# Performance work log

Measured on AMD Instinct MI355X. Metric: run time of the kernel, lower is better.

## Reference

```python
import jax, jax.numpy as jnp
import numpy as np

B, T, U = 4, 500, 100
D = 512   # d_model
H = 512   # d_hidden
L = 2     # num_layers
V = 64    # len(phonemes)


def setup_inputs() -> dict:
    key = jax.random.key(0)
    ks = jax.random.split(key, 14)
    g = lambda k, shp: (jax.random.normal(k, shp, jnp.float32) * 0.05)
    return {
        "input_ids": jax.random.randint(ks[0], (B, U), 0, V),
        "memory": jax.random.normal(ks[1], (B, T, D), jnp.float32),
        "emb": g(ks[2], (V, D)),
        # stacked per-layer LSTM params (torch layout: [4H, in], gate order i,f,g,o)
        "w_ih": g(ks[3], (L, 4 * H, D)),
        "w_hh": g(ks[4], (L, 4 * H, H)),
        "b_ih": g(ks[5], (L, 4 * H)),
        "b_hh": g(ks[6], (L, 4 * H)),
        "fc_w": g(ks[7], (D, H)),     # torch Linear [out, in]
        "fc_b": g(ks[8], (D,)),
        "jw1": g(ks[9], (H, 2 * D)),  # Joint.forward_layer
        "jb1": g(ks[10], (H,)),
        "jw2": g(ks[11], (V, H)),     # Joint.project_layer
        "jb2": g(ks[12], (V,)),
    }


def _lstm_layer(x, wi, wh, bi, bh):
    # x: [B, U, in] -> returns ([B, U, H], h_T [B,H], c_T [B,H])
    b = x.shape[0]
    h0 = jnp.zeros((b, H), x.dtype)
    c0 = jnp.zeros((b, H), x.dtype)
    bias = bi + bh

    def step(carry, xt):
        h, c = carry
        gates = xt @ wi.T + h @ wh.T + bias  # [B, 4H]
        i, f, g, o = jnp.split(gates, 4, axis=-1)
        c = jax.nn.sigmoid(f) * c + jax.nn.sigmoid(i) * jnp.tanh(g)
        h = jax.nn.sigmoid(o) * jnp.tanh(c)
        return (h, c), h

    (hT, cT), ys = jax.lax.scan(step, (h0, c0), jnp.swapaxes(x, 0, 1))
    return jnp.swapaxes(ys, 0, 1), hT, cT


def reference(input_ids, memory, emb, w_ih, w_hh, b_ih, b_hh, fc_w, fc_b, jw1, jb1, jw2, jb2):
    # embedding lookup
    x = emb[input_ids]  # [B, U, D]
    hs, cs = [], []
    for l in range(L):
        x, hT, cT = _lstm_layer(x, w_ih[l], w_hh[l], b_ih[l], b_hh[l])
        hs.append(hT)
        cs.append(cT)
    h = jnp.stack(hs)  # [L, B, H]
    c = jnp.stack(cs)
    x = x @ fc_w.T + fc_b  # [B, U, D]

    # Joint: linear over concat(enc, dec) == split-weight broadcast add (same math)
    we = jw1[:, :D]  # acts on enc_state
    wd = jw1[:, D:]  # acts on dec_state
    enc_p = jnp.einsum("btd,hd->bth", memory, we)  # [B, T, H]
    dec_p = jnp.einsum("bud,hd->buh", x, wd)       # [B, U, H]
    joint_h = jnp.tanh(enc_p[:, :, None, :] + dec_p[:, None, :, :] + jb1)  # [B,T,U,H]
    out = jnp.einsum("btuh,vh->btuv", joint_h, jw2) + jb2  # [B, T, U, V]
    return out, h, c
```

## Files before the change

### kernel.cpp

```cpp
#include <hip/hip_runtime.h>

#define Bc 4
#define Tc 500
#define Uc 100
#define Vc 64
#define G4 2048

typedef __attribute__((ext_vector_type(8))) short short8v;
typedef __attribute__((ext_vector_type(4))) float f32x4;
typedef _Float16 h2v __attribute__((ext_vector_type(2)));

#define SMEM_BYTES 86016

__device__ __forceinline__ float fsig(float x) {
  return __builtin_amdgcn_rcpf(1.f + __expf(-x));
}
__device__ __forceinline__ float ftanh(float x) {
  float e = __expf(2.f * x);
  return 1.f - 2.f * __builtin_amdgcn_rcpf(e + 1.f);
}
__device__ __forceinline__ short f2bf(float f) {
  unsigned u = __float_as_uint(f);
  unsigned r = (u + 0x7FFFu + ((u >> 16) & 1u)) >> 16;
  return (short)r;
}

__device__ __forceinline__ unsigned ldA(const unsigned* p) {
  return __hip_atomic_load(p, __ATOMIC_RELAXED, __HIP_MEMORY_SCOPE_AGENT);
}
__device__ __forceinline__ void stA(unsigned* p, unsigned v) {
  __hip_atomic_store(p, v, __ATOMIC_RELAXED, __HIP_MEMORY_SCOPE_AGENT);
}

template <int ATOMICST>
__device__ __forceinline__ void gemm_tile(
    char* smem,
    const float* __restrict__ A, int lda,
    const float* __restrict__ Bw, int ldb,
    const float* __restrict__ bias, const float* __restrict__ bias2,
    float* __restrict__ C, int ldc, int N, int m0, int n0,
    const int* __restrict__ ids, const float* __restrict__ emb)
{
  float (*As)[65] = (float (*)[65])smem;
  float (*Bs)[65] = (float (*)[65])(smem + 4160);
  const int tid = threadIdx.x;
  const int tx = tid & 15, ty = tid >> 4;
  float acc[4][4] = {};
  for (int k0 = 0; k0 < 512; k0 += 16) {
#pragma unroll
    for (int i = 0; i < 4; ++i) {
      int n = n0 + ty + 16 * i;
      float av = 0.f;
      if (n < N) {
        const float* ar = ids ? (emb + (long)ids[n] * 512) : (A + (long)n * lda);
        av = ar[k0 + tx];
      }
      As[tx][ty + 16 * i] = av;
      Bs[tx][ty + 16 * i] = Bw[(long)(m0 + ty + 16 * i) * ldb + k0 + tx];
    }
    __syncthreads();
#pragma unroll
    for (int kl = 0; kl < 16; ++kl) {
      float a[4], b[4];
#pragma unroll
      for (int i = 0; i < 4; ++i) a[i] = As[kl][ty * 4 + i];
#pragma unroll
      for (int j = 0; j < 4; ++j) b[j] = Bs[kl][tx * 4 + j];
#pragma unroll
      for (int i = 0; i < 4; ++i)
#pragma unroll
        for (int j = 0; j < 4; ++j) acc[i][j] += a[i] * b[j];
    }
    __syncthreads();
  }
#pragma unroll
  for (int i = 0; i < 4; ++i) {
    int n = n0 + ty * 4 + i;
    if (n >= N) continue;
#pragma unroll
    for (int j = 0; j < 4; ++j) {
      int m = m0 + tx * 4 + j;
      float v = acc[i][j];
      if (bias)  v += bias[m];
      if (bias2) v += bias2[m];
      if (ATOMICST)
        stA((unsigned*)C + (long)n * ldc + m, __float_as_uint(v));
      else
        C[(long)n * ldc + m] = v;
    }
  }
}

__device__ void wdc_tile(char* smem,
                         const float* __restrict__ jw1,
                         const float* __restrict__ fc_w,
                         float* __restrict__ wdc, int n0, int m0)
{
  float (*As)[65] = (float (*)[65])smem;
  float (*Bs)[65] = (float (*)[65])(smem + 4160);
  const int tid = threadIdx.x;
  const int tx = tid & 15, ty = tid >> 4;
  float acc[4][4] = {};
  for (int k0 = 0; k0 < 512; k0 += 16) {
#pragma unroll
    for (int i = 0; i < 4; ++i) {
      As[tx][ty + 16 * i] = jw1[(long)(n0 + ty + 16 * i) * 1024 + 512 + k0 + tx];
      Bs[ty][tx + 16 * i] = fc_w[(long)(k0 + ty) * 512 + m0 + tx + 16 * i];
    }
    __syncthreads();
#pragma unroll
    for (int kl = 0; kl < 16; ++kl) {
      float a[4], b[4];
#pragma unroll
      for (int i = 0; i < 4; ++i) a[i] = As[kl][ty * 4 + i];
#pragma unroll
      for (int j = 0; j < 4; ++j) b[j] = Bs[kl][tx * 4 + j];
#pragma unroll
      for (int i = 0; i < 4; ++i)
#pragma unroll
        for (int j = 0; j < 4; ++j) acc[i][j] += a[i] * b[j];
    }
    __syncthreads();
  }
#pragma unroll
  for (int i = 0; i < 4; ++i)
#pragma unroll
    for (int j = 0; j < 4; ++j)
      stA((unsigned*)wdc + (long)(n0 + ty * 4 + i) * 512 + m0 + tx * 4 + j,
          __float_as_uint(acc[i][j]));
}

__device__ void dec_tile(char* smem,
                         const float* __restrict__ h1s, const float* __restrict__ wdc,
                         const float* __restrict__ jw1, const float* __restrict__ fc_b,
                         const float* __restrict__ jb1, float* __restrict__ decb,
                         const int* __restrict__ f1, int m0, int n0)
{
  float (*As)[65] = (float (*)[65])smem;
  float (*Bs)[65] = (float (*)[65])(smem + 4160);
  float* biasl = (float*)(smem + 8320);
  const int tid = threadIdx.x;
  const int tx = tid & 15, ty = tid >> 4;
  int u_hi = 0;
  for (int rr = 0; rr < 64; ++rr) {
    int r = n0 + rr;
    if (r < 400) { int u = r % Uc; u_hi = max(u_hi, u + 1); }
  }
  if (tid < 32)
    while ((int)ldA((const unsigned*)(f1 + tid * 16)) < u_hi)
      __builtin_amdgcn_s_sleep(8);
  if (tid < 64) {
    int m = m0 + tid;
    const float4* wp = (const float4*)(jw1 + (long)m * 1024 + 512);
    const float4* fb = (const float4*)fc_b;
    float bb = jb1[m];
#pragma unroll 8
    for (int d4 = 0; d4 < 128; ++d4) {
      float4 w = wp[d4], f = fb[d4];
      bb += w.x * f.x + w.y * f.y + w.z * f.z + w.w * f.w;
    }
    biasl[tid] = bb;
  }
  __syncthreads();
  const unsigned* h1u = (const unsigned*)h1s;
  const unsigned* wdu = (const unsigned*)wdc;
  float acc[4][4] = {};
  for (int k0 = 0; k0 < 512; k0 += 16) {
    unsigned uA[4], uB[4];
#pragma unroll
    for (int i = 0; i < 4; ++i) {
      int n = n0 + ty + 16 * i;
      uA[i] = (n < 400) ? ldA(h1u + (long)(n % Uc) * G4 + (n / Uc) * 512 + k0 + tx) : 0u;
      uB[i] = ldA(wdu + (long)(m0 + ty + 16 * i) * 512 + k0 + tx);
    }
#pragma unroll
    for (int i = 0; i < 4; ++i) {
      int n = n0 + ty + 16 * i;
      while (uA[i] == 0xFFFFFFFFu)
        uA[i] = ldA(h1u + (long)(n % Uc) * G4 + (n / Uc) * 512 + k0 + tx);
      while (uB[i] == 0xFFFFFFFFu)
        uB[i] = ldA(wdu + (long)(m0 + ty + 16 * i) * 512 + k0 + tx);
      As[tx][ty + 16 * i] = __uint_as_float(uA[i]);
      Bs[tx][ty + 16 * i] = __uint_as_float(uB[i]);
    }
    __syncthreads();
#pragma unroll
    for (int kl = 0; kl < 16; ++kl) {
      float a[4], b[4];
#pragma unroll
      for (int i = 0; i < 4; ++i) a[i] = As[kl][ty * 4 + i];
#pragma unroll
      for (int j = 0; j < 4; ++j) b[j] = Bs[kl][tx * 4 + j];
#pragma unroll
      for (int i = 0; i < 4; ++i)
#pragma unroll
        for (int j = 0; j < 4; ++j) acc[i][j] += a[i] * b[j];
    }
    __syncthreads();
  }
#pragma unroll
  for (int i = 0; i < 4; ++i) {
    int n = n0 + ty * 4 + i;
    if (n >= 400) continue;
#pragma unroll
    for (int j = 0; j < 4; ++j)
      stA((unsigned*)decb + (long)n * 512 + m0 + tx * 4 + j,
          __float_as_uint(acc[i][j] + biasl[tx * 4 + j]));
  }
}

__device__ void rec_path(
    char* smem, int role,
    const float* __restrict__ ixp0,
    const float* __restrict__ wih1, const float* __restrict__ whh0,
    const float* __restrict__ whh1,
    const float* __restrict__ bih1, const float* __restrict__ bhh1,
    unsigned* __restrict__ h0s16, unsigned* __restrict__ h1s16,
    float* __restrict__ h1s32,
    float* __restrict__ hO, float* __restrict__ cO, int* __restrict__ flags)
{
  unsigned* hl = (unsigned*)smem;
  float4* red4 = (float4*)(smem + 8192);
  const int tid = threadIdx.x;
  const bool isL1 = role >= 16;
  const int jb = role - 16;
  const int rg = tid & 15, ks = tid >> 4;
  const int lane = tid & 63, wv = tid >> 6;
  int* f1 = flags + 512;

  h2v wr[8][16];
#pragma unroll
  for (int r = 0; r < 8; ++r) {
    int lr = rg * 8 + r;
    const float* wsrc; int grow;
    if (!isL1) { int q = lr >> 5, uu = lr & 31; grow = q * 512 + role * 32 + uu; wsrc = whh0; }
    else {
      if (lr < 64) { int q = lr >> 4, uu = lr & 15; grow = q * 512 + jb * 16 + uu; wsrc = wih1; }
      else { int l2 = lr - 64; int q = l2 >> 4, uu = l2 & 15; grow = q * 512 + jb * 16 + uu; wsrc = whh1; }
    }
    const float* wp = wsrc + (long)grow * 512 + ks * 32;
#pragma unroll
    for (int jj = 0; jj < 16; ++jj) {
      h2v t; t[0] = (_Float16)wp[2 * jj]; t[1] = (_Float16)wp[2 * jj + 1];
      wr[r][jj] = t;
    }
  }

  const int npair = isL1 ? 8 : 16;
  const bool eact = tid < npair * 4;
  const int ep = tid >> 2, eb = tid & 3;
  float creg[2] = {0.f, 0.f};
  float bgate[2][4];
  if (isL1 && eact) {
#pragma unroll
    for (int o = 0; o < 2; ++o)
#pragma unroll
      for (int q = 0; q < 4; ++q) {
        int grow = q * 512 + jb * 16 + 2 * ep + o;
        bgate[o][q] = bih1[grow] + bhh1[grow];
      }
  }

  const unsigned* ixu = (const unsigned*)ixp0;
  const int hsrc = (isL1 && rg >= 8) ? 1 : 0;
  const float* redf = (const float*)red4;

  unsigned ixn[8];
  const unsigned* ib0 = (!isL1 && eact)
      ? ixu + ((long)(eb * Uc) * G4 + role * 32 + 2 * ep) : nullptr;
  if (ib0) {
#pragma unroll
    for (int o = 0; o < 2; ++o)
#pragma unroll
      for (int q = 0; q < 4; ++q) ixn[o * 4 + q] = ldA(ib0 + o + q * 512);
  }

  for (int s = 0; s < Uc; ++s) {
    unsigned ha[4] = {0u, 0u, 0u, 0u}, hb[4] = {0u, 0u, 0u, 0u};
    const unsigned* pa = nullptr; const unsigned* pb = nullptr;
    if (!isL1) { if (s > 0) pa = h0s16 + (long)(s - 1) * 1024 + tid * 4; }
    else {
      pa = h0s16 + (long)s * 1024 + tid * 4;
      if (s > 0) pb = h1s16 + (long)(s - 1) * 1024 + tid * 4;
    }
    if (pa) {
#pragma unroll
      for (int c = 0; c < 4; ++c) ha[c] = ldA(pa + c);
    }
    if (pb) {
#pragma unroll
      for (int c = 0; c < 4; ++c) hb[c] = ldA(pb + c);
    }

    float ixv[2][4] = {};
    if (ib0) {
      const unsigned* ib = ib0 + (long)s * G4;
#pragma unroll
      for (int o = 0; o < 2; ++o)
#pragma unroll
        for (int q = 0; q < 4; ++q) {
          unsigned g = ixn[o * 4 + q];
          while (g == 0xFFFFFFFFu) { __builtin_amdgcn_s_sleep(1); g = ldA(ib + o + q * 512); }
          ixv[o][q] = __uint_as_float(g);
        }
    }

    if (pa) {
#pragma unroll
      for (int c = 0; c < 4; ++c)
        while (ha[c] == 0xFFFFFFFFu) { __builtin_amdgcn_s_sleep(1); ha[c] = ldA(pa + c); }
    }
    if (pb) {
#pragma unroll
      for (int c = 0; c < 4; ++c)
        while (hb[c] == 0xFFFFFFFFu) { __builtin_amdgcn_s_sleep(1); hb[c] = ldA(pb + c); }
    }

    if (ib0 && s + 1 < Uc) {
      const unsigned* ibn = ib0 + (long)(s + 1) * G4;
#pragma unroll
      for (int o = 0; o < 2; ++o)
#pragma unroll
        for (int q = 0; q < 4; ++q) ixn[o * 4 + q] = ldA(ibn + o + q * 512);
    }

    *(uint4*)&hl[tid * 4] = make_uint4(ha[0], ha[1], ha[2], ha[3]);
    if (isL1)
      *(uint4*)&hl[1024 + tid * 4] = make_uint4(hb[0], hb[1], hb[2], hb[3]);
    __syncthreads();

    float acc[8][4] = {};
    const unsigned* hbase = &hl[hsrc * 1024 + ks * 16];
#pragma unroll
    for (int jw = 0; jw < 4; ++jw) {
      unsigned q[4][4];
#pragma unroll
      for (int b = 0; b < 4; ++b) {
        uint4 t = *(const uint4*)&hbase[b * 256 + jw * 4];
        q[b][0] = t.x; q[b][1] = t.y; q[b][2] = t.z; q[b][3] = t.w;
      }
#pragma unroll
      for (int r = 0; r < 8; ++r)
#pragma unroll
        for (int w = 0; w < 4; ++w) {
          h2v wv2 = wr[r][jw * 4 + w];
#pragma unroll
          for (int b = 0; b < 4; ++b)
            acc[r][b] = __builtin_amdgcn_fdot2(
                wv2, __builtin_bit_cast(h2v, q[b][w]), acc[r][b], false);
        }
    }
#pragma unroll
    for (int r = 0; r < 8; ++r)
#pragma unroll
      for (int b = 0; b < 4; ++b) {
        float v = acc[r][b];
        v += __shfl_xor(v, 16);
        v += __shfl_xor(v, 32);
        acc[r][b] = v;
      }
    if (lane < 16) {
#pragma unroll
      for (int r = 0; r < 8; ++r)
        red4[wv * 128 + lane * 8 + r] =
            make_float4(acc[r][0], acc[r][1], acc[r][2], acc[r][3]);
    }
    __syncthreads();

    if (eact) {
      float hn2[2], cn2[2];
#pragma unroll
      for (int o = 0; o < 2; ++o) {
        int uu = 2 * ep + o;
        float gv[4];
#pragma unroll
        for (int q = 0; q < 4; ++q) {
          int lrA = isL1 ? (q * 16 + uu) : (q * 32 + uu);
          float sv = 0.f;
#pragma unroll
          for (int w = 0; w < 4; ++w)
            sv += redf[(w * 128 + (lrA >> 3) * 8 + (lrA & 7)) * 4 + eb];
          if (isL1) {
            int lrB = 64 + q * 16 + uu;
#pragma unroll
            for (int w = 0; w < 4; ++w)
              sv += redf[(w * 128 + (lrB >> 3) * 8 + (lrB & 7)) * 4 + eb];
            sv += bgate[o][q];
          } else {
            sv += ixv[o][q];
          }
          gv[q] = sv;
        }
        float cn = fsig(gv[1]) * creg[o] + fsig(gv[0]) * ftanh(gv[2]);
        float hn = fsig(gv[3]) * ftanh(cn);
        creg[o] = cn;
        hn2[o] = hn; cn2[o] = cn;
      }
      int gu = (isL1 ? jb * 16 : role * 32) + 2 * ep;
      h2v hp; hp[0] = (_Float16)hn2[0]; hp[1] = (_Float16)hn2[1];
      unsigned pw = __builtin_bit_cast(unsigned, hp);
      stA((isL1 ? h1s16 : h0s16) + (long)s * 1024 + eb * 256 + (gu >> 1), pw);
      if (isL1) {
        unsigned* d32 = (unsigned*)h1s32 + (long)s * G4 + eb * 512 + gu;
        stA(d32, __float_as_uint(hn2[0]));
        stA(d32 + 1, __float_as_uint(hn2[1]));
      }
      if (s == Uc - 1) {
#pragma unroll
        for (int o = 0; o < 2; ++o) {
          hO[(isL1 ? G4 : 0) + eb * 512 + gu + o] = hn2[o];
          cO[(isL1 ? G4 : 0) + eb * 512 + gu + o] = cn2[o];
        }
      }
      if (isL1 && tid == 0) stA((unsigned*)(f1 + jb * 16), (unsigned)(s + 1));
    }
  }
}

__global__ __launch_bounds__(256, 1) void k_fused(
    const int* __restrict__ ids, const float* __restrict__ emb,
    const float* __restrict__ memory,
    const float* __restrict__ w_ih, const float* __restrict__ b_ih,
    const float* __restrict__ b_hh,
    const float* __restrict__ wih1, const float* __restrict__ whh0,
    const float* __restrict__ whh1,
    const float* __restrict__ bih1, const float* __restrict__ bhh1,
    const float* __restrict__ jw1, const float* __restrict__ jb1,
    const float* __restrict__ fc_w, const float* __restrict__ fc_b,
    float* __restrict__ ixp0, unsigned* __restrict__ h0s16,
    unsigned* __restrict__ h1s16, float* __restrict__ h1s32,
    float* __restrict__ wdc, float* __restrict__ decb, float* __restrict__ encb,
    float* __restrict__ hO, float* __restrict__ cO, int* __restrict__ flags)
{
  __shared__ __attribute__((aligned(16))) char smem[SMEM_BYTES];
  const int blk = blockIdx.x;
  if (blk < 48) {
    rec_path(smem, blk, ixp0, wih1, whh0, whh1, bih1, bhh1,
             h0s16, h1s16, h1s32, hO, cO, flags);
    return;
  }
  const int w = blk - 48;
  static const int nt_ord[7] = {0, 1, 3, 4, 2, 5, 6};
  for (int k = 0; k < 3; ++k) {
    int t = w + 208 * k;
    if (t >= 600) break;
    if (k) __syncthreads();
    if (t < 224) {
      gemm_tile<1>(smem, nullptr, 0, w_ih, 512, b_ih, b_hh,
                   ixp0, G4, Bc * Uc, (t % 32) * 64, nt_ord[t / 32] * 64, ids, emb);
    } else if (t < 288) {
      int g = t - 224;
      wdc_tile(smem, jw1, fc_w, wdc, (g & 7) * 64, (g >> 3) * 64);
    } else if (t < 544) {
      int g = t - 288;
      gemm_tile<0>(smem, memory, 512, jw1, 1024, nullptr, nullptr,
                   encb, 512, Bc * Tc, (g & 7) * 64, (g >> 3) * 64, nullptr, nullptr);
    } else {
      int g = t - 544;
      dec_tile(smem, h1s32, wdc, jw1, fc_b, jb1, decb, flags + 512,
               (g & 7) * 64, (g >> 3) * 64);
    }
  }
}

__global__ __launch_bounds__(256) void k_jmfma(
    const float* __restrict__ enc, const float* __restrict__ dec,
    const float* __restrict__ jw2, const float* __restrict__ jb2,
    float* __restrict__ out)
{
  __shared__ float el[512];
  __shared__ short th[112][136];
  const int tid = threadIdx.x;
  const int lane = tid & 63, wv = tid >> 6;
  const int bt = blockIdx.x;
  const int b = bt / Tc;
  const int v0 = wv * 16;
  const int vl = lane & 15, kg = lane >> 4;

  short8v breg[16];
#pragma unroll
  for (int ksx = 0; ksx < 16; ++ksx) {
    const float* wp = jw2 + (long)(v0 + vl) * 512 + ksx * 32 + kg * 8;
    float4 x0 = *(const float4*)wp;
    float4 x1 = *(const float4*)(wp + 4);
    short8v t;
    t[0] = f2bf(x0.x); t[1] = f2bf(x0.y); t[2] = f2bf(x0.z); t[3] = f2bf(x0.w);
    t[4] = f2bf(x1.x); t[5] = f2bf(x1.y); t[6] = f2bf(x1.z); t[7] = f2bf(x1.w);
    breg[ksx] = t;
  }
  const float jbv = jb2[v0 + vl];
  for (int i = tid; i < 512; i += 256) el[i] = enc[(long)bt * 512 + i];

  f32x4 acc[7];
#pragma unroll
  for (int ut = 0; ut < 7; ++ut) acc[ut] = (f32x4){0.f, 0.f, 0.f, 0.f};
  __syncthreads();

  const float* dec0 = dec + (long)b * Uc * 512;
  for (int kc = 0; kc < 4; ++kc) {
#pragma unroll 5
    for (int it = 0; it < 50; ++it) {
      int flat = it * 256 + tid;
      int u = flat >> 7, kk = flat & 127;
      float dv = dec0[(long)u * 512 + kc * 128 + kk];
      th[u][kk] = f2bf(ftanh(el[kc * 128 + kk] + dv));
    }
    __syncthreads();
#pragma unroll
    for (int ks4 = 0; ks4 < 4; ++ks4) {
      int ko = ks4 * 32 + kg * 8;
#pragma unroll
      for (int ut = 0; ut < 7; ++ut) {
        short8v a = *(const short8v*)&th[ut * 16 + vl][ko];
        acc[ut] = __builtin_amdgcn_mfma_f32_16x16x32_bf16(a, breg[kc * 4 + ks4],
                                                          acc[ut], 0, 0, 0);
      }
    }
    __syncthreads();
  }
#pragma unroll
  for (int ut = 0; ut < 7; ++ut) {
#pragma unroll
    for (int i = 0; i < 4; ++i) {
      int u = ut * 16 + kg * 4 + i;
      if (u < Uc)
        out[((long)bt * Uc + u) * 64 + v0 + vl] = acc[ut][i] + jbv;
    }
  }
}

extern "C" void kernel_launch(void* const* d_in, const int* in_sizes, int n_in,
                              void* d_out, int out_size, void* d_ws, size_t ws_size,
                              hipStream_t stream)
{
  const int*   ids    = (const int*)d_in[0];
  const float* memory = (const float*)d_in[1];
  const float* emb    = (const float*)d_in[2];
  const float* w_ih   = (const float*)d_in[3];
  const float* w_hh   = (const float*)d_in[4];
  const float* b_ih   = (const float*)d_in[5];
  const float* b_hh   = (const float*)d_in[6];
  const float* fc_w   = (const float*)d_in[7];
  const float* fc_b   = (const float*)d_in[8];
  const float* jw1    = (const float*)d_in[9];
  const float* jb1    = (const float*)d_in[10];
  const float* jw2    = (const float*)d_in[11];
  const float* jb2    = (const float*)d_in[12];
  float* out = (float*)d_out;

  float* wsf = (float*)d_ws;
  int*      flags = (int*)d_ws;
  float*    ixp0  = wsf + 4096;
  unsigned* h0s16 = (unsigned*)(wsf + 823296);
  unsigned* h1s16 = (unsigned*)(wsf + 925696);
  float*    h1s32 = wsf + 1028096;
  float*    wdc   = wsf + 1232896;
  float*    decb  = wsf + 1495040;
  float*    encb  = wsf + 1699840;

  float* hO = out + (long)Bc * Tc * Uc * Vc;
  float* cO = hO + 2 * Bc * 512;

  hipMemsetAsync(flags, 0, 4096 * 4, stream);
  hipMemsetAsync(ixp0, 0xFF, (size_t)(1699840 - 4096) * 4, stream);

  k_fused<<<256, 256, 0, stream>>>(ids, emb, memory,
                                   w_ih, b_ih, b_hh,
                                   w_ih + (long)G4 * 512,
                                   w_hh,
                                   w_hh + (long)G4 * 512,
                                   b_ih + G4, b_hh + G4,
                                   jw1, jb1, fc_w, fc_b,
                                   ixp0, h0s16, h1s16, h1s32, wdc, decb, encb,
                                   hO, cO, flags);

  k_jmfma<<<2000, 256, 0, stream>>>(encb, decb, jw2, jb2, out);
}
```

Baseline: 706.7 us.

## Fuse joint projection into persistent kernel with counter-based dataflow sync

Removes the separate joint MFMA kernel and runs the joint tanh+projection inside the worker blocks of the fused persistent kernel. Per-row-group completion counters for the encoder and decoder projections let joint work start as soon as its inputs are ready, overlapping with the recurrent LSTM path. Each block now loops over 2000/208 (b,t) rows and processes u-tiles one at a time with one accumulator, giving up the 7-way MFMA batching. It also enlarges the sentinel memset and adds per-element spin checks.

```diff
diff --git a/kernel.cpp b/kernel.cpp
--- a/kernel.cpp
+++ b/kernel.cpp
@@ -30,6 +30,9 @@
 }
 __device__ __forceinline__ void stA(unsigned* p, unsigned v) {
   __hip_atomic_store(p, v, __ATOMIC_RELAXED, __HIP_MEMORY_SCOPE_AGENT);
+}
+__device__ __forceinline__ void ctrBump(int* c) {
+  __hip_atomic_fetch_add(c, 1, __ATOMIC_RELAXED, __HIP_MEMORY_SCOPE_AGENT);
 }
 
 template <int ATOMICST>
@@ -39,7 +42,8 @@
     const float* __restrict__ Bw, int ldb,
     const float* __restrict__ bias, const float* __restrict__ bias2,
     float* __restrict__ C, int ldc, int N, int m0, int n0,
-    const int* __restrict__ ids, const float* __restrict__ emb)
+    const int* __restrict__ ids, const float* __restrict__ emb,
+    int* __restrict__ ctr)
 {
   float (*As)[65] = (float (*)[65])smem;
   float (*Bs)[65] = (float (*)[65])(smem + 4160);
@@ -88,6 +92,10 @@
       else
         C[(long)n * ldc + m] = v;
     }
+  }
+  if (ctr) {
+    __syncthreads();
+    if (tid == 0) ctrBump(ctr);
   }
 }
 
@@ -134,7 +142,8 @@
                          const float* __restrict__ h1s, const float* __restrict__ wdc,
                          const float* __restrict__ jw1, const float* __restrict__ fc_b,
                          const float* __restrict__ jb1, float* __restrict__ decb,
-                         const int* __restrict__ f1, int m0, int n0)
+                         const int* __restrict__ f1, int* __restrict__ dctr,
+                         int m0, int n0)
 {
   float (*As)[65] = (float (*)[65])smem;
   float (*Bs)[65] = (float (*)[65])(smem + 4160);
@@ -206,6 +215,95 @@
     for (int j = 0; j < 4; ++j)
       stA((unsigned*)decb + (long)n * 512 + m0 + tx * 4 + j,
           __float_as_uint(acc[i][j] + biasl[tx * 4 + j]));
+  }
+  __syncthreads();
+  if (tid == 0) ctrBump(dctr);
+}
+
+__device__ void joint_path(char* smem, int w,
+    const float* __restrict__ encb, const float* __restrict__ decb,
+    const float* __restrict__ jw2, const float* __restrict__ jb2,
+    float* __restrict__ out,
+    const int* __restrict__ enc_ctr, const int* __restrict__ dec_ctr)
+{
+  float* el = (float*)smem;
+  short (*th)[136] = (short (*)[136])(smem + 2048);
+  const int tid = threadIdx.x;
+  const int lane = tid & 63, wvx = tid >> 6;
+  const int v0 = wvx * 16;
+  const int vl = lane & 15, kg = lane >> 4;
+
+  short8v breg[16];
+#pragma unroll
+  for (int ksx = 0; ksx < 16; ++ksx) {
+    const float* wp = jw2 + (long)(v0 + vl) * 512 + ksx * 32 + kg * 8;
+    float4 x0 = *(const float4*)wp;
+    float4 x1 = *(const float4*)(wp + 4);
+    short8v t;
+    t[0] = f2bf(x0.x); t[1] = f2bf(x0.y); t[2] = f2bf(x0.z); t[3] = f2bf(x0.w);
+    t[4] = f2bf(x1.x); t[5] = f2bf(x1.y); t[6] = f2bf(x1.z); t[7] = f2bf(x1.w);
+    breg[ksx] = t;
+  }
+  const float jbv = jb2[v0 + vl];
+
+  for (int bt = w; bt < Bc * Tc; bt += 208) {
+    const int b = bt / Tc;
+    if (tid == 0)
+      while ((int)ldA((const unsigned*)(enc_ctr + (bt >> 6) * 16)) < 8)
+        __builtin_amdgcn_s_sleep(16);
+    __syncthreads();
+    for (int i = tid; i < 512; i += 256) {
+      const unsigned* ep = (const unsigned*)(encb + (long)bt * 512 + i);
+      unsigned g = *ep;
+      while (g == 0xFFFFFFFFu) { __builtin_amdgcn_s_sleep(1); g = ldA(ep); }
+      el[i] = __uint_as_float(g);
+    }
+    __syncthreads();
+    const float* dec0 = decb + (long)b * Uc * 512;
+
+    for (int ut = 0; ut < 7; ++ut) {
+      if (tid == 0) {
+        int ulo = ut * 16, uhi = min(Uc - 1, ut * 16 + 15);
+        for (int bb2 = 0; bb2 < 4; ++bb2) {
+          int glo = (bb2 * Uc + ulo) >> 6, ghi = (bb2 * Uc + uhi) >> 6;
+          for (int g = glo; g <= ghi; ++g)
+            while ((int)ldA((const unsigned*)(dec_ctr + g * 16)) < 8)
+              __builtin_amdgcn_s_sleep(16);
+        }
+      }
+      __syncthreads();
+      f32x4 acc = (f32x4){0.f, 0.f, 0.f, 0.f};
+      for (int kc = 0; kc < 4; ++kc) {
+#pragma unroll
+        for (int it = 0; it < 8; ++it) {
+          int flat = it * 256 + tid;
+          int ul = flat >> 7, kk = flat & 127;
+          int u = ut * 16 + ul;
+          float v = 0.f;
+          if (u < Uc) {
+            const unsigned* dp = (const unsigned*)(dec0 + (long)u * 512 + kc * 128 + kk);
+            unsigned g = *dp;
+            while (g == 0xFFFFFFFFu) { __builtin_amdgcn_s_sleep(1); g = ldA(dp); }
+            v = ftanh(el[kc * 128 + kk] + __uint_as_float(g));
+          }
+          th[ul][kk] = f2bf(v);
+        }
+        __syncthreads();
+#pragma unroll
+        for (int ks4 = 0; ks4 < 4; ++ks4) {
+          short8v a = *(const short8v*)&th[vl][ks4 * 32 + kg * 8];
+          acc = __builtin_amdgcn_mfma_f32_16x16x32_bf16(a, breg[kc * 4 + ks4],
+                                                        acc, 0, 0, 0);
+        }
+        __syncthreads();
+      }
+#pragma unroll
+      for (int i = 0; i < 4; ++i) {
+        int u = ut * 16 + kg * 4 + i;
+        if (u < Uc)
+          out[((long)bt * Uc + u) * 64 + v0 + vl] = acc[i] + jbv;
+      }
+    }
   }
 }
 
@@ -427,13 +525,17 @@
     const float* __restrict__ bih1, const float* __restrict__ bhh1,
     const float* __restrict__ jw1, const float* __restrict__ jb1,
     const float* __restrict__ fc_w, const float* __restrict__ fc_b,
+    const float* __restrict__ jw2, const float* __restrict__ jb2,
     float* __restrict__ ixp0, unsigned* __restrict__ h0s16,
     unsigned* __restrict__ h1s16, float* __restrict__ h1s32,
     float* __restrict__ wdc, float* __restrict__ decb, float* __restrict__ encb,
+    float* __restrict__ out,
     float* __restrict__ hO, float* __restrict__ cO, int* __restrict__ flags)
 {
   __shared__ __attribute__((aligned(16))) char smem[SMEM_BYTES];
   const int blk = blockIdx.x;
+  int* dec_ctr = flags + 1536;
+  int* enc_ctr = flags + 2048;
   if (blk < 48) {
     rec_path(smem, blk, ixp0, wih1, whh0, whh1, bih1, bhh1,
              h0s16, h1s16, h1s32, hO, cO, flags);
@@ -447,86 +549,24 @@
     if (k) __syncthreads();
     if (t < 224) {
       gemm_tile<1>(smem, nullptr, 0, w_ih, 512, b_ih, b_hh,
-                   ixp0, G4, Bc * Uc, (t % 32) * 64, nt_ord[t / 32] * 64, ids, emb);
+                   ixp0, G4, Bc * Uc, (t % 32) * 64, nt_ord[t / 32] * 64,
+                   ids, emb, nullptr);
     } else if (t < 288) {
       int g = t - 224;
       wdc_tile(smem, jw1, fc_w, wdc, (g & 7) * 64, (g >> 3) * 64);
     } else if (t < 544) {
       int g = t - 288;
-      gemm_tile<0>(smem, memory, 512, jw1, 1024, nullptr, nullptr,
-                   encb, 512, Bc * Tc, (g & 7) * 64, (g >> 3) * 64, nullptr, nullptr);
+      gemm_tile<1>(smem, memory, 512, jw1, 1024, nullptr, nullptr,
+                   encb, 512, Bc * Tc, (g & 7) * 64, (g >> 3) * 64,
+                   nullptr, nullptr, enc_ctr + (g >> 3) * 16);
     } else {
       int g = t - 544;
       dec_tile(smem, h1s32, wdc, jw1, fc_b, jb1, decb, flags + 512,
-               (g & 7) * 64, (g >> 3) * 64);
-    }
-  }
-}
-
-__global__ __launch_bounds__(256) void k_jmfma(
-    const float* __restrict__ enc, const float* __restrict__ dec,
-    const float* __restrict__ jw2, const float* __restrict__ jb2,
-    float* __restrict__ out)
-{
-  __shared__ float el[512];
-  __shared__ short th[112][136];
-  const int tid = threadIdx.x;
-  const int lane = tid & 63, wv = tid >> 6;
-  const int bt = blockIdx.x;
-  const int b = bt / Tc;
-  const int v0 = wv * 16;
-  const int vl = lane & 15, kg = lane >> 4;
-
-  short8v breg[16];
-#pragma unroll
-  for (int ksx = 0; ksx < 16; ++ksx) {
-    const float* wp = jw2 + (long)(v0 + vl) * 512 + ksx * 32 + kg * 8;
-    float4 x0 = *(const float4*)wp;
-    float4 x1 = *(const float4*)(wp + 4);
-    short8v t;
-    t[0] = f2bf(x0.x); t[1] = f2bf(x0.y); t[2] = f2bf(x0.z); t[3] = f2bf(x0.w);
-    t[4] = f2bf(x1.x); t[5] = f2bf(x1.y); t[6] = f2bf(x1.z); t[7] = f2bf(x1.w);
-    breg[ksx] = t;
-  }
-  const float jbv = jb2[v0 + vl];
-  for (int i = tid; i < 512; i += 256) el[i] = enc[(long)bt * 512 + i];
-
-  f32x4 acc[7];
-#pragma unroll
-  for (int ut = 0; ut < 7; ++ut) acc[ut] = (f32x4){0.f, 0.f, 0.f, 0.f};
+               dec_ctr + (g >> 3) * 16, (g & 7) * 64, (g >> 3) * 64);
+    }
+  }
   __syncthreads();
-
-  const float* dec0 = dec + (long)b * Uc * 512;
-  for (int kc = 0; kc < 4; ++kc) {
-#pragma unroll 5
-    for (int it = 0; it < 50; ++it) {
-      int flat = it * 256 + tid;
-      int u = flat >> 7, kk = flat & 127;
-      float dv = dec0[(long)u * 512 + kc * 128 + kk];
-      th[u][kk] = f2bf(ftanh(el[kc * 128 + kk] + dv));
-    }
-    __syncthreads();
-#pragma unroll
-    for (int ks4 = 0; ks4 < 4; ++ks4) {
-      int ko = ks4 * 32 + kg * 8;
-#pragma unroll
-      for (int ut = 0; ut < 7; ++ut) {
-        short8v a = *(const short8v*)&th[ut * 16 + vl][ko];
-        acc[ut] = __builtin_amdgcn_mfma_f32_16x16x32_bf16(a, breg[kc * 4 + ks4],
-                                                          acc[ut], 0, 0, 0);
-      }
-    }
-    __syncthreads();
-  }
-#pragma unroll
-  for (int ut = 0; ut < 7; ++ut) {
-#pragma unroll
-    for (int i = 0; i < 4; ++i) {
-      int u = ut * 16 + kg * 4 + i;
-      if (u < Uc)
-        out[((long)bt * Uc + u) * 64 + v0 + vl] = acc[ut][i] + jbv;
-    }
-  }
+  joint_path(smem, w, encb, decb, jw2, jb2, out, enc_ctr, dec_ctr);
 }
 
 extern "C" void kernel_launch(void* const* d_in, const int* in_sizes, int n_in,
@@ -562,7 +602,7 @@
   float* cO = hO + 2 * Bc * 512;
 
   hipMemsetAsync(flags, 0, 4096 * 4, stream);
-  hipMemsetAsync(ixp0, 0xFF, (size_t)(1699840 - 4096) * 4, stream);
+  hipMemsetAsync(ixp0, 0xFF, (size_t)(2723840 - 4096) * 4, stream);
 
   k_fused<<<256, 256, 0, stream>>>(ids, emb, memory,
                                    w_ih, b_ih, b_hh,
@@ -570,9 +610,7 @@
                                    w_hh,
                                    w_hh + (long)G4 * 512,
                                    b_ih + G4, b_hh + G4,
-                                   jw1, jb1, fc_w, fc_b,
+                                   jw1, jb1, fc_w, fc_b, jw2, jb2,
                                    ixp0, h0s16, h1s16, h1s32, wdc, decb, encb,
-                                   hO, cO, flags);
-
-  k_jmfma<<<2000, 256, 0, stream>>>(encb, decb, jw2, jb2, out);
-}
+                                   out, hO, cO, flags);
+}
```

Result: slower. 1.177 ms (+66.5%).
